# Optimization experiments

Measured on AMD Instinct MI355X. Metric: run time of the kernel, lower is better.

## Reference

```python
import jax, jax.numpy as jnp
import numpy as np
from jax import lax

J2 = -1.0
J4 = 0.5
KT = 0.5
DT = 0.01
SIGMA = float(np.sqrt(2.0 * KT * DT))  # noise scale per Euler-Maruyama step


def setup_inputs() -> dict:
    key = jax.random.key(0)
    k_x, = jax.random.split(key, 1)
    n_samples, n_dim = 2048, 256
    x0 = jax.random.normal(k_x, (n_samples, n_dim), dtype=jnp.float32)
    b = jnp.zeros((n_dim,), dtype=jnp.float32)  # learned bias parameter
    return {"x0": x0, "b": b, "n_steps": 500}


def reference(x0, b, n_steps):
    # Langevin dynamics: x <- x - grad_V(x)*dt + sqrt(2 kT dt)*N(0,1)
    # grad_V(x) = 2*J2*x + 4*J4*x^3 + b
    keys = jax.random.split(jax.random.key(1), n_steps)

    def step(x, k):
        grad = 2.0 * J2 * x + 4.0 * J4 * x * x * x + b
        noise = jax.random.normal(k, x.shape, x.dtype) * SIGMA
        return x - grad * DT + noise, None

    x, _ = lax.scan(step, x0, keys)
    return x
```

## Files before the change

### kernel.cpp

```cpp
#include <hip/hip_runtime.h>


__device__ __forceinline__ void tf2x32(unsigned k0, unsigned k1,
                                       unsigned c0, unsigned c1,
                                       unsigned& o0, unsigned& o1) {
  const unsigned k2 = k0 ^ k1 ^ 0x1BD11BDAu;
  unsigned x0 = c0 + k0, x1 = c1 + k1;
#define TF1(R) x0 += x1; x1 = ((x1 << (R)) | (x1 >> (32 - (R)))); x1 ^= x0;
  TF1(13) TF1(15) TF1(26) TF1(6)  x0 += k1; x1 += k2 + 1u;
  TF1(17) TF1(29) TF1(16) TF1(24) x0 += k2; x1 += k0 + 2u;
  TF1(13) TF1(15) TF1(26) TF1(6)  x0 += k0; x1 += k1 + 3u;
  TF1(17) TF1(29) TF1(16) TF1(24) x0 += k1; x1 += k2 + 4u;
  TF1(13) TF1(15) TF1(26) TF1(6)  x0 += k2; x1 += k0 + 5u;
#undef TF1
  o0 = x0; o1 = x1;
}

__device__ __forceinline__ void tf_fold2(const unsigned w[8],
                                         unsigned ca, unsigned cb,
                                         unsigned& ra, unsigned& rb) {
  unsigned a0 = w[0], a1 = ca + w[1];
  unsigned b0 = w[0], b1 = cb + w[1];
#define TFR2(R)                                   \
  a0 += a1; b0 += b1;                             \
  a1 = ((a1 << (R)) | (a1 >> (32 - (R)))) ^ a0;   \
  b1 = ((b1 << (R)) | (b1 >> (32 - (R)))) ^ b0;
#define TFINJ2(i0, i1) a0 += w[i0]; b0 += w[i0]; a1 += w[i1]; b1 += w[i1];
  TFR2(13) TFR2(15) TFR2(26) TFR2(6)  TFINJ2(1, 3)
  TFR2(17) TFR2(29) TFR2(16) TFR2(24) TFINJ2(2, 4)
  TFR2(13) TFR2(15) TFR2(26) TFR2(6)  TFINJ2(0, 5)
  TFR2(17) TFR2(29) TFR2(16) TFR2(24) TFINJ2(1, 6)
  TFR2(13) TFR2(15) TFR2(26) TFR2(6)  TFINJ2(2, 7)
#undef TFR2
#undef TFINJ2
  ra = a0 ^ a1;
  rb = b0 ^ b1;
}

__device__ __forceinline__ void b2n2(unsigned bba, unsigned bbb,
                                     float& na, float& nb) {
  const float fa = __uint_as_float((bba >> 9) | 0x3F800000u) - 1.0f;
  const float fb = __uint_as_float((bbb >> 9) | 0x3F800000u) - 1.0f;
  const float ua = fmaf(fa, 2.0f, -0.99999994f);
  const float ub = fmaf(fb, 2.0f, -0.99999994f);
  const float ma = ua * ua, mb = ub * ub;
  const float la = __log2f(1.0f - ma);
  const float lb = __log2f(1.0f - mb);
  const float wa = fmaf(la, -0.69314718246459961f, la * 1.9046543e-09f);
  const float wb = fmaf(lb, -0.69314718246459961f, lb * 1.9046543e-09f);
  const bool sa = wa < 5.0f, sb = wb < 5.0f;
  const float za = sa ? (wa - 2.5f) : (__builtin_amdgcn_sqrtf(wa) - 3.0f);
  const float zb = sb ? (wb - 2.5f) : (__builtin_amdgcn_sqrtf(wb) - 3.0f);
  float pa =           sa ? 2.81022636e-08f  : -0.000200214257f;
  float pb =           sb ? 2.81022636e-08f  : -0.000200214257f;
  pa = fmaf(pa, za,    sa ? 3.43273939e-07f  :  0.000100950558f);
  pb = fmaf(pb, zb,    sb ? 3.43273939e-07f  :  0.000100950558f);
  pa = fmaf(pa, za,    sa ? -3.5233877e-06f  :  0.00134934322f);
  pb = fmaf(pb, zb,    sb ? -3.5233877e-06f  :  0.00134934322f);
  pa = fmaf(pa, za,    sa ? -4.39150654e-06f : -0.00367342844f);
  pb = fmaf(pb, zb,    sb ? -4.39150654e-06f : -0.00367342844f);
  pa = fmaf(pa, za,    sa ? 0.00021858087f   :  0.00573950773f);
  pb = fmaf(pb, zb,    sb ? 0.00021858087f   :  0.00573950773f);
  pa = fmaf(pa, za,    sa ? -0.00125372503f  : -0.0076224613f);
  pb = fmaf(pb, zb,    sb ? -0.00125372503f  : -0.0076224613f);
  pa = fmaf(pa, za,    sa ? -0.00417768164f  :  0.00943887047f);
  pb = fmaf(pb, zb,    sb ? -0.00417768164f  :  0.00943887047f);
  pa = fmaf(pa, za,    sa ? 0.246640727f     :  1.00167406f);
  pb = fmaf(pb, zb,    sb ? 0.246640727f     :  1.00167406f);
  pa = fmaf(pa, za,    sa ? 1.50140941f      :  2.83297682f);
  pb = fmaf(pb, zb,    sb ? 1.50140941f      :  2.83297682f);
  na = __uint_as_float(0x3FB504F3u) * (pa * ua);
  nb = __uint_as_float(0x3FB504F3u) * (pb * ub);
}

__global__ __launch_bounds__(256, 4) void langevin_tf(
    const float* __restrict__ x0p, const float* __restrict__ bias,
    const int* __restrict__ nsteps_p, float* __restrict__ out,
    int H, int ndim) {
  __shared__ __align__(16) unsigned skeys[513 * 8];
  const int n_steps = __builtin_amdgcn_readfirstlane(nsteps_p[0]);
  const int nfill = n_steps < 512 ? n_steps : 512;
  for (int l = (int)threadIdx.x; l < nfill; l += (int)blockDim.x) {
    unsigned o0, o1;
    tf2x32(0u, 1u, 0u, (unsigned)l, o0, o1);
    const unsigned k2 = o0 ^ o1 ^ 0x1BD11BDAu;
    unsigned* wp = &skeys[8 * l];
    wp[0] = o0;       wp[1] = o1;       wp[2] = k2;       wp[3] = k2 + 1u;
    wp[4] = o0 + 2u;  wp[5] = o1 + 3u;  wp[6] = k2 + 4u;  wp[7] = o0 + 5u;
  }
  __syncthreads();

  const int j = (int)(blockIdx.x * blockDim.x + threadIdx.x);
  if (j >= H) return;
  const unsigned ca = (unsigned)j;
  const unsigned cb = (unsigned)(j + H);
  float xa = x0p[j];
  float xb = x0p[j + H];
  const float ba = bias[j % ndim];
  const float bb = bias[(j + H) % ndim];

  if (n_steps <= 512) {
    const uint4* sk4 = (const uint4*)skeys;
    uint4 klo = sk4[0], khi = sk4[1];
#pragma unroll 1
    for (int t = 0; t < n_steps; ++t) {
      const uint4 nlo = sk4[2 * t + 2];
      const uint4 nhi = sk4[2 * t + 3];
      const unsigned w[8] = {klo.x, klo.y, klo.z, klo.w,
                             khi.x, khi.y, khi.z, khi.w};
      unsigned ra, rb;
      tf_fold2(w, ca, cb, ra, rb);
      float na, nb;
      b2n2(ra, rb, na, nb);
      const float ga = -2.0f * xa + ((2.0f * xa) * xa) * xa + ba;
      const float gb = -2.0f * xb + ((2.0f * xb) * xb) * xb + bb;
      xa = (xa - ga * 0.01f) + na * 0.1f;
      xb = (xb - gb * 0.01f) + nb * 0.1f;
      klo = nlo; khi = nhi;
    }
  } else {
    for (int t = 0; t < n_steps; ++t) {
      unsigned o0, o1;
      tf2x32(0u, 1u, 0u, (unsigned)t, o0, o1);
      const unsigned k2 = o0 ^ o1 ^ 0x1BD11BDAu;
      const unsigned w[8] = {o0, o1, k2, k2 + 1u, o0 + 2u, o1 + 3u,
                             k2 + 4u, o0 + 5u};
      unsigned ra, rb;
      tf_fold2(w, ca, cb, ra, rb);
      float na, nb;
      b2n2(ra, rb, na, nb);
      const float ga = -2.0f * xa + ((2.0f * xa) * xa) * xa + ba;
      const float gb = -2.0f * xb + ((2.0f * xb) * xb) * xb + bb;
      xa = (xa - ga * 0.01f) + na * 0.1f;
      xb = (xb - gb * 0.01f) + nb * 0.1f;
    }
  }
  out[j] = xa;
  out[j + H] = xb;
}

extern "C" void kernel_launch(void* const* d_in, const int* in_sizes, int n_in,
                              void* d_out, int out_size, void* d_ws, size_t ws_size,
                              hipStream_t stream) {
  (void)n_in; (void)d_ws; (void)ws_size; (void)out_size;
  const float* x0 = (const float*)d_in[0];
  const float* b = (const float*)d_in[1];
  const int* ns = (const int*)d_in[2];
  float* out = (float*)d_out;

  const int n = in_sizes[0];
  const int ndim = in_sizes[1];
  const int H = n / 2;
  const int block = 256;
  const int grid = (H + block - 1) / block;
  hipLaunchKernelGGL(langevin_tf, dim3(grid), dim3(block), 0, stream,
                     x0, b, ns, out, H, ndim);
}
```

Baseline: 654.3 us.

## Assign one element per thread and pair consecutive timesteps for ILP

Each thread now owns a single element instead of two, which doubles the grid. It gets two-way instruction-level parallelism by evaluating the threefry hashes for two consecutive timesteps together, then applying the two Euler updates in sequence. The launch-bounds occupancy hint goes from 4 to 8. The log-to-ln conversion is reduced to a single multiply, which can change rounding slightly relative to the split-constant form. Twice as many threads each do the same amount of work, so the total work is unchanged; the change trades per-thread register pressure for more waves in flight.

```diff
diff --git a/kernel.cpp b/kernel.cpp
--- a/kernel.cpp
+++ b/kernel.cpp
@@ -16,16 +16,16 @@
   o0 = x0; o1 = x1;
 }
 
-__device__ __forceinline__ void tf_fold2(const unsigned w[8],
-                                         unsigned ca, unsigned cb,
-                                         unsigned& ra, unsigned& rb) {
-  unsigned a0 = w[0], a1 = ca + w[1];
-  unsigned b0 = w[0], b1 = cb + w[1];
+__device__ __forceinline__ void tf_fold2k(const unsigned wa[8],
+                                          const unsigned wb[8], unsigned cj,
+                                          unsigned& ra, unsigned& rb) {
+  unsigned a0 = wa[0], a1 = cj + wa[1];
+  unsigned b0 = wb[0], b1 = cj + wb[1];
 #define TFR2(R)                                   \
   a0 += a1; b0 += b1;                             \
   a1 = ((a1 << (R)) | (a1 >> (32 - (R)))) ^ a0;   \
   b1 = ((b1 << (R)) | (b1 >> (32 - (R)))) ^ b0;
-#define TFINJ2(i0, i1) a0 += w[i0]; b0 += w[i0]; a1 += w[i1]; b1 += w[i1];
+#define TFINJ2(i0, i1) a0 += wa[i0]; b0 += wb[i0]; a1 += wa[i1]; b1 += wb[i1];
   TFR2(13) TFR2(15) TFR2(26) TFR2(6)  TFINJ2(1, 3)
   TFR2(17) TFR2(29) TFR2(16) TFR2(24) TFINJ2(2, 4)
   TFR2(13) TFR2(15) TFR2(26) TFR2(6)  TFINJ2(0, 5)
@@ -46,8 +46,8 @@
   const float ma = ua * ua, mb = ub * ub;
   const float la = __log2f(1.0f - ma);
   const float lb = __log2f(1.0f - mb);
-  const float wa = fmaf(la, -0.69314718246459961f, la * 1.9046543e-09f);
-  const float wb = fmaf(lb, -0.69314718246459961f, lb * 1.9046543e-09f);
+  const float wa = la * -0.693147180559945f;
+  const float wb = lb * -0.693147180559945f;
   const bool sa = wa < 5.0f, sb = wb < 5.0f;
   const float za = sa ? (wa - 2.5f) : (__builtin_amdgcn_sqrtf(wa) - 3.0f);
   const float zb = sb ? (wb - 2.5f) : (__builtin_amdgcn_sqrtf(wb) - 3.0f);
@@ -73,11 +73,11 @@
   nb = __uint_as_float(0x3FB504F3u) * (pb * ub);
 }
 
-__global__ __launch_bounds__(256, 4) void langevin_tf(
+__global__ __launch_bounds__(256, 8) void langevin_tf(
     const float* __restrict__ x0p, const float* __restrict__ bias,
     const int* __restrict__ nsteps_p, float* __restrict__ out,
-    int H, int ndim) {
-  __shared__ __align__(16) unsigned skeys[513 * 8];
+    int N, int ndim) {
+  __shared__ __align__(16) unsigned skeys[512 * 8];
   const int n_steps = __builtin_amdgcn_readfirstlane(nsteps_p[0]);
   const int nfill = n_steps < 512 ? n_steps : 512;
   for (int l = (int)threadIdx.x; l < nfill; l += (int)blockDim.x) {
@@ -91,52 +91,66 @@
   __syncthreads();
 
   const int j = (int)(blockIdx.x * blockDim.x + threadIdx.x);
-  if (j >= H) return;
-  const unsigned ca = (unsigned)j;
-  const unsigned cb = (unsigned)(j + H);
-  float xa = x0p[j];
-  float xb = x0p[j + H];
-  const float ba = bias[j % ndim];
-  const float bb = bias[(j + H) % ndim];
+  if (j >= N) return;
+  const unsigned cj = (unsigned)j;
+  float x = x0p[j];
+  const float b = bias[j % ndim];
 
   if (n_steps <= 512) {
     const uint4* sk4 = (const uint4*)skeys;
-    uint4 klo = sk4[0], khi = sk4[1];
+    int t = 0;
 #pragma unroll 1
-    for (int t = 0; t < n_steps; ++t) {
-      const uint4 nlo = sk4[2 * t + 2];
-      const uint4 nhi = sk4[2 * t + 3];
-      const unsigned w[8] = {klo.x, klo.y, klo.z, klo.w,
-                             khi.x, khi.y, khi.z, khi.w};
+    for (; t + 1 < n_steps; t += 2) {
+      const uint4 a_lo = sk4[2 * t + 0], a_hi = sk4[2 * t + 1];
+      const uint4 b_lo = sk4[2 * t + 2], b_hi = sk4[2 * t + 3];
+      const unsigned wa[8] = {a_lo.x, a_lo.y, a_lo.z, a_lo.w,
+                              a_hi.x, a_hi.y, a_hi.z, a_hi.w};
+      const unsigned wb[8] = {b_lo.x, b_lo.y, b_lo.z, b_lo.w,
+                              b_hi.x, b_hi.y, b_hi.z, b_hi.w};
       unsigned ra, rb;
-      tf_fold2(w, ca, cb, ra, rb);
+      tf_fold2k(wa, wb, cj, ra, rb);
       float na, nb;
       b2n2(ra, rb, na, nb);
-      const float ga = -2.0f * xa + ((2.0f * xa) * xa) * xa + ba;
-      const float gb = -2.0f * xb + ((2.0f * xb) * xb) * xb + bb;
-      xa = (xa - ga * 0.01f) + na * 0.1f;
-      xb = (xb - gb * 0.01f) + nb * 0.1f;
-      klo = nlo; khi = nhi;
+      float g = -2.0f * x + ((2.0f * x) * x) * x + b;
+      x = (x - g * 0.01f) + na * 0.1f;
+      g = -2.0f * x + ((2.0f * x) * x) * x + b;
+      x = (x - g * 0.01f) + nb * 0.1f;
+    }
+    if (t < n_steps) {
+      const uint4 a_lo = sk4[2 * t + 0], a_hi = sk4[2 * t + 1];
+      const unsigned wa[8] = {a_lo.x, a_lo.y, a_lo.z, a_lo.w,
+                              a_hi.x, a_hi.y, a_hi.z, a_hi.w};
+      unsigned ra, rb;
+      tf_fold2k(wa, wa, cj, ra, rb);
+      float na, nb;
+      b2n2(ra, ra, na, nb);
+      const float g = -2.0f * x + ((2.0f * x) * x) * x + b;
+      x = (x - g * 0.01f) + na * 0.1f;
     }
   } else {
-    for (int t = 0; t < n_steps; ++t) {
-      unsigned o0, o1;
-      tf2x32(0u, 1u, 0u, (unsigned)t, o0, o1);
-      const unsigned k2 = o0 ^ o1 ^ 0x1BD11BDAu;
-      const unsigned w[8] = {o0, o1, k2, k2 + 1u, o0 + 2u, o1 + 3u,
-                             k2 + 4u, o0 + 5u};
+    for (int t = 0; t < n_steps; t += 2) {
+      unsigned oa0, oa1, ob0, ob1;
+      tf2x32(0u, 1u, 0u, (unsigned)t, oa0, oa1);
+      tf2x32(0u, 1u, 0u, (unsigned)(t + 1), ob0, ob1);
+      const unsigned ka2 = oa0 ^ oa1 ^ 0x1BD11BDAu;
+      const unsigned kb2 = ob0 ^ ob1 ^ 0x1BD11BDAu;
+      const unsigned wa[8] = {oa0, oa1, ka2, ka2 + 1u, oa0 + 2u, oa1 + 3u,
+                              ka2 + 4u, oa0 + 5u};
+      const unsigned wb[8] = {ob0, ob1, kb2, kb2 + 1u, ob0 + 2u, ob1 + 3u,
+                              kb2 + 4u, ob0 + 5u};
       unsigned ra, rb;
-      tf_fold2(w, ca, cb, ra, rb);
+      tf_fold2k(wa, wb, cj, ra, rb);
       float na, nb;
       b2n2(ra, rb, na, nb);
-      const float ga = -2.0f * xa + ((2.0f * xa) * xa) * xa + ba;
-      const float gb = -2.0f * xb + ((2.0f * xb) * xb) * xb + bb;
-      xa = (xa - ga * 0.01f) + na * 0.1f;
-      xb = (xb - gb * 0.01f) + nb * 0.1f;
+      float g = -2.0f * x + ((2.0f * x) * x) * x + b;
+      x = (x - g * 0.01f) + na * 0.1f;
+      if (t + 1 < n_steps) {
+        g = -2.0f * x + ((2.0f * x) * x) * x + b;
+        x = (x - g * 0.01f) + nb * 0.1f;
+      }
     }
   }
-  out[j] = xa;
-  out[j + H] = xb;
+  out[j] = x;
 }
 
 extern "C" void kernel_launch(void* const* d_in, const int* in_sizes, int n_in,
@@ -150,9 +164,8 @@
 
   const int n = in_sizes[0];
   const int ndim = in_sizes[1];
-  const int H = n / 2;
   const int block = 256;
-  const int grid = (H + block - 1) / block;
+  const int grid = (n + block - 1) / block;
   hipLaunchKernelGGL(langevin_tf, dim3(grid), dim3(block), 0, stream,
-                     x0, b, ns, out, H, ndim);
+                     x0, b, ns, out, n, ndim);
 }
```

After: 593.1 us. -9.3%, faster.
